# Optimization experiments

Measured on AMD Instinct MI355X. Metric: run time of the kernel, lower is better.

## Reference

```python
import jax, jax.numpy as jnp
import numpy as np

GROUPS = 4
RATIO = 2


def setup_inputs() -> dict:
    key = jax.random.key(0)
    k1, k2, k3 = jax.random.split(key, 3)
    B, C, H, W = 16, 256, 64, 64
    c_out = 2 * GROUPS * RATIO ** 2  # 32
    x = jax.random.normal(k1, (B, C, H, W), dtype=jnp.float32)
    # offset conv: normal_init std=0.001 (full 1x1 conv)
    w_off = jax.random.normal(k2, (c_out, C), dtype=jnp.float32) * 0.001
    b_off = jnp.zeros((c_out,), dtype=jnp.float32)
    # scope conv: grouped 1x1 (groups=4); init is zeros in the module, use tiny
    # random values so sigmoid != exactly 0.5 and the path is exercised
    w_scope = jax.random.normal(k3, (GROUPS, c_out // GROUPS, C // GROUPS), dtype=jnp.float32) * 0.001
    b_scope = jnp.zeros((c_out,), dtype=jnp.float32)
    return {"x": x, "w_off": w_off, "b_off": b_off, "w_scope": w_scope, "b_scope": b_scope}


def _pixel_shuffle(t, r):
    B, C, H, W = t.shape
    Co = C // (r * r)
    t = t.reshape(B, Co, r, r, H, W)
    t = t.transpose(0, 1, 4, 2, 5, 3)  # B, Co, H, r, W, r
    return t.reshape(B, Co, H * r, W * r)


def _bilinear_border(img, ix, iy):
    # img: (c, H, W); ix, iy: (Ho, Wo) pixel coords in input space
    c, H, W = img.shape
    ix = jnp.clip(ix, 0.0, W - 1.0)  # border padding: clamp coordinate
    iy = jnp.clip(iy, 0.0, H - 1.0)
    x0f = jnp.floor(ix)
    y0f = jnp.floor(iy)
    wx = ix - x0f
    wy = iy - y0f
    x0 = jnp.clip(x0f.astype(jnp.int32), 0, W - 1)
    x1 = jnp.clip(x0 + 1, 0, W - 1)
    y0 = jnp.clip(y0f.astype(jnp.int32), 0, H - 1)
    y1 = jnp.clip(y0 + 1, 0, H - 1)
    v00 = img[:, y0, x0]
    v01 = img[:, y0, x1]
    v10 = img[:, y1, x0]
    v11 = img[:, y1, x1]
    return (v00 * (1 - wy) * (1 - wx) + v01 * (1 - wy) * wx
            + v10 * wy * (1 - wx) + v11 * wy * wx)


def reference(x, w_off, b_off, w_scope, b_scope):
    B, C, H, W = x.shape
    g, r = GROUPS, RATIO
    # offset 1x1 conv
    off = jnp.einsum('bihw,oi->bohw', x, w_off) + b_off[None, :, None, None]
    # grouped scope 1x1 conv + sigmoid scaling
    xgc = x.reshape(B, g, C // g, H, W)
    sc = jnp.einsum('bgihw,goi->bgohw', xgc, w_scope).reshape(B, -1, H, W)
    sc = sc + b_scope[None, :, None, None]
    off = jax.nn.sigmoid(sc) * 0.5 * off
    # pixel shuffle to (B, 2*g, Ho, Wo)
    off = _pixel_shuffle(off, r)
    Ho, Wo = H * r, W * r
    # rearrange: x 'b (c grp) h w -> (b grp) c h w'; offset 'b (grp two) h w -> (b grp) h w two'
    cg = C // g
    xg = x.reshape(B, cg, g, H, W).transpose(0, 2, 1, 3, 4).reshape(B * g, cg, H, W)
    og = off.reshape(B, g, 2, Ho, Wo).transpose(0, 1, 3, 4, 2).reshape(B * g, Ho, Wo, 2)
    # sampling grid: centers + offset, normalized by (Wo, Ho), align_corners=False
    posx = jnp.linspace(0.5, Wo - 0.5, Wo, dtype=x.dtype)[None, :]   # (1, Wo)
    posy = jnp.linspace(0.5, Ho - 0.5, Ho, dtype=x.dtype)[:, None]   # (Ho, 1)
    gx = 2.0 * (posx + og[..., 0]) / Wo - 1.0  # (B*g, Ho, Wo)
    gy = 2.0 * (posy + og[..., 1]) / Ho - 1.0
    # unnormalize (align_corners=False): pix = ((g+1)*size - 1) / 2
    ix = ((gx + 1.0) * W - 1.0) * 0.5
    iy = ((gy + 1.0) * H - 1.0) * 0.5
    out = jax.vmap(_bilinear_border)(xg, ix, iy)  # (B*g, cg, Ho, Wo)
    # rearrange back: '(b grp) c h w -> b (c grp) h w'
    out = out.reshape(B, g, cg, Ho, Wo).transpose(0, 2, 1, 3, 4).reshape(B, C, Ho, Wo)
    return out
```

## Files before the change

### kernel.cpp

```cpp
#include <hip/hip_runtime.h>
#include <math.h>

#define B_   16
#define C_   256
#define H_   64
#define W_   64
#define G_   4
#define HO_  128
#define WO_  128
#define HW_  (H_ * W_)
#define HOWO_ (HO_ * WO_)

__global__ __launch_bounds__(256) void prep_kernel(
    const float* __restrict__ w_off,
    const float* __restrict__ w_scope,
    float* __restrict__ wcomb)
{
    const int k = blockIdx.x * 256 + threadIdx.x;
    if (k >= 4 * 64 * 40) return;
    const int q = k % 40;
    const int r = k / 40;
    const int i2 = r & 63;
    const int t  = r >> 6;
    float v;
    if (q < 32) v = w_off[q * 256 + t * 64 + i2];
    else        v = w_scope[t * 512 + (q - 32) * 64 + i2];
    wcomb[k] = v;
}

__global__ __launch_bounds__(256) void fused_kernel(
    const float* __restrict__ x,
    const float* __restrict__ wcomb,
    const float* __restrict__ b_off,
    const float* __restrict__ b_scope,
    float* __restrict__ out)
{
    __shared__ float red[4 * 64 * 32];
    __shared__ float2 coords[4 * 2 * 128];

    const int tid = threadIdx.x;
    const int t = __builtin_amdgcn_readfirstlane(tid >> 6);
    const int w = tid & 63;
    const int h = blockIdx.x & 63;
    const int b = blockIdx.x >> 6;

    const float* xq = x + (size_t)b * C_ * HW_ + (size_t)t * 64 * HW_ +
                      h * W_ + w;
    const float* wt = wcomb + t * (64 * 40);

    float aoff[32];
    float asc[8];
#pragma unroll
    for (int o = 0; o < 32; ++o) aoff[o] = 0.f;
#pragma unroll
    for (int o = 0; o < 8; ++o) asc[o] = 0.f;

#pragma unroll 2
    for (int i2 = 0; i2 < 64; ++i2) {
        const float xv = xq[(size_t)i2 * HW_];
        const float* wr = wt + i2 * 40;
#pragma unroll
        for (int o = 0; o < 32; ++o) aoff[o] += xv * wr[o];
#pragma unroll
        for (int j = 0; j < 8; ++j)  asc[j] += xv * wr[32 + j];
    }

    {
        float4* rw = (float4*)&red[(t * 64 + w) * 32];
#pragma unroll
        for (int j = 0; j < 8; ++j) {
            rw[(j + w) & 7] = make_float4(aoff[4 * j + 0], aoff[4 * j + 1],
                                          aoff[4 * j + 2], aoff[4 * j + 3]);
        }
    }
    __syncthreads();

    float4 s0 = make_float4(0.f, 0.f, 0.f, 0.f);
    float4 s1 = make_float4(0.f, 0.f, 0.f, 0.f);
#pragma unroll
    for (int tt = 0; tt < 4; ++tt) {
        const float4* rr = (const float4*)&red[(tt * 64 + w) * 32];
        const float4 a = rr[(2 * t + 0 + w) & 7];
        const float4 c = rr[(2 * t + 1 + w) & 7];
        s0.x += a.x; s0.y += a.y; s0.z += a.z; s0.w += a.w;
        s1.x += c.x; s1.y += c.y; s1.z += c.z; s1.w += c.w;
    }

    float f[8];
    {
        float ao[8] = {s0.x, s0.y, s0.z, s0.w, s1.x, s1.y, s1.z, s1.w};
#pragma unroll
        for (int j = 0; j < 8; ++j) {
            const float offv = ao[j] + b_off[8 * t + j];
            const float scv  = asc[j] + b_scope[8 * t + j];
            const float sg   = 1.f / (1.f + expf(-scv));
            f[j] = sg * 0.5f * offv;
        }
    }

#pragma unroll
    for (int r1 = 0; r1 < 2; ++r1) {
        float c2[4];
#pragma unroll
        for (int r2 = 0; r2 < 2; ++r2) {
            const int ho = 2 * h + r1;
            const int wo = 2 * w + r2;
            float ix = ((float)wo - 0.5f + f[2 * r1 + r2]) * 0.5f;
            float iy = ((float)ho - 0.5f + f[4 + 2 * r1 + r2]) * 0.5f;
            ix = fminf(fmaxf(ix, 0.f), (float)(W_ - 1));
            iy = fminf(fmaxf(iy, 0.f), (float)(H_ - 1));
            c2[2 * r2 + 0] = ix;
            c2[2 * r2 + 1] = iy;
        }
        float4* cw = (float4*)&coords[t * 256 + r1 * 128 + 2 * w];
        *cw = make_float4(c2[0], c2[1], c2[2], c2[3]);
    }

    __syncthreads();

    const int wo = tid & 127;
    const int z  = tid >> 7;
    const int ho = 2 * h + z;

    const float* xb0 = x + (size_t)b * C_ * HW_;
    float* ob0 = out + (size_t)b * C_ * HOWO_ + ho * WO_ + wo;

#pragma unroll
    for (int g = 0; g < 4; ++g) {
        const float2 c = coords[g * 256 + z * 128 + wo];
        const float ix = c.x, iy = c.y;

        const float x0f = floorf(ix);
        const float y0f = floorf(iy);
        const float wx = ix - x0f;
        const float wy = iy - y0f;
        int x0 = (int)x0f;
        int y0 = (int)y0f;
        x0 = max(0, min(x0, W_ - 1));
        y0 = max(0, min(y0, H_ - 1));
        const int x1 = min(x0 + 1, W_ - 1);
        const int y1 = min(y0 + 1, H_ - 1);

        const float w00 = (1.f - wy) * (1.f - wx);
        const float w01 = (1.f - wy) * wx;
        const float w10 = wy * (1.f - wx);
        const float w11 = wy * wx;

        const int p00 = y0 * W_ + x0;
        const int p01 = y0 * W_ + x1;
        const int p10 = y1 * W_ + x0;
        const int p11 = y1 * W_ + x1;

        const float* xb = xb0 + (size_t)g * HW_;
        float* ob = ob0 + (size_t)g * HOWO_;

#pragma unroll 4
        for (int cc = 0; cc < 64; ++cc) {
            const float* pl = xb + (size_t)cc * 4 * HW_;
            const float v = pl[p00] * w00 + pl[p01] * w01 +
                            pl[p10] * w10 + pl[p11] * w11;
            ob[(size_t)cc * 4 * HOWO_] = v;
        }
    }
}

extern "C" void kernel_launch(void* const* d_in, const int* in_sizes, int n_in,
                              void* d_out, int out_size, void* d_ws, size_t ws_size,
                              hipStream_t stream) {
    const float* x       = (const float*)d_in[0];
    const float* w_off   = (const float*)d_in[1];
    const float* b_off   = (const float*)d_in[2];
    const float* w_scope = (const float*)d_in[3];
    const float* b_scope = (const float*)d_in[4];
    float* out = (float*)d_out;
    float* wcomb = (float*)d_ws;

    prep_kernel<<<dim3(40), 256, 0, stream>>>(w_off, w_scope, wcomb);
    fused_kernel<<<dim3(B_ * H_), 256, 0, stream>>>(
        x, wcomb, b_off, b_scope, out);
}
```

Baseline: 93.94 us.

## Split fused kernel into conv and sampling kernels with global coords buffer

Splits the fused conv+sample kernel into three launches: weight prep, a conv kernel that writes sampling coordinates to global workspace, and a separate sample kernel with a 3D grid over (row pair, group, batch). The conv kernel drops the shared-memory cross-wave reduction. Each wave now reads all 256 input channels for its own 8 offset outputs, which quadruples x reads in the conv stage instead of using an LDS reduction. The sample kernel has one group per block, giving more, smaller blocks for latency hiding. The cost is an extra launch and a global round trip for the coordinates.

```diff
diff --git a/kernel.cpp b/kernel.cpp
--- a/kernel.cpp
+++ b/kernel.cpp
@@ -17,85 +17,72 @@
     float* __restrict__ wcomb)
 {
     const int k = blockIdx.x * 256 + threadIdx.x;
-    if (k >= 4 * 64 * 40) return;
-    const int q = k % 40;
-    const int r = k / 40;
-    const int i2 = r & 63;
-    const int t  = r >> 6;
+    const int q = k & 15;
+    const int i = (k >> 4) & 255;
+    const int t = k >> 12;
     float v;
-    if (q < 32) v = w_off[q * 256 + t * 64 + i2];
-    else        v = w_scope[t * 512 + (q - 32) * 64 + i2];
+    if (q < 8) {
+        v = w_off[(8 * t + q) * 256 + i];
+    } else {
+        const int i2 = i - 64 * t;
+        v = (i2 >= 0 && i2 < 64) ? w_scope[t * 512 + (q - 8) * 64 + i2] : 0.f;
+    }
     wcomb[k] = v;
 }
 
-__global__ __launch_bounds__(256) void fused_kernel(
+__global__ __launch_bounds__(256) void conv_kernel(
     const float* __restrict__ x,
     const float* __restrict__ wcomb,
     const float* __restrict__ b_off,
     const float* __restrict__ b_scope,
-    float* __restrict__ out)
+    float2* __restrict__ coords)
 {
-    __shared__ float red[4 * 64 * 32];
-    __shared__ float2 coords[4 * 2 * 128];
-
     const int tid = threadIdx.x;
     const int t = __builtin_amdgcn_readfirstlane(tid >> 6);
     const int w = tid & 63;
     const int h = blockIdx.x & 63;
     const int b = blockIdx.x >> 6;
 
-    const float* xq = x + (size_t)b * C_ * HW_ + (size_t)t * 64 * HW_ +
-                      h * W_ + w;
-    const float* wt = wcomb + t * (64 * 40);
+    const float* xrow = x + (size_t)b * C_ * HW_ + h * W_ + w;
+    const float* wt = wcomb + t * (256 * 16);
 
-    float aoff[32];
-    float asc[8];
+    float off[8];
+    float sc[8];
 #pragma unroll
-    for (int o = 0; o < 32; ++o) aoff[o] = 0.f;
+    for (int j = 0; j < 8; ++j) { off[j] = 0.f; sc[j] = 0.f; }
+
 #pragma unroll
-    for (int o = 0; o < 8; ++o) asc[o] = 0.f;
-
-#pragma unroll 2
-    for (int i2 = 0; i2 < 64; ++i2) {
-        const float xv = xq[(size_t)i2 * HW_];
-        const float* wr = wt + i2 * 40;
+    for (int seg = 0; seg < 4; ++seg) {
+        const float* xs = xrow + (size_t)seg * 64 * HW_;
+        const float* ws = wt + seg * 64 * 16;
+        if (seg == t) {
+#pragma unroll 4
+            for (int i2 = 0; i2 < 64; ++i2) {
+                const float xv = xs[(size_t)i2 * HW_];
+                const float* wr = ws + i2 * 16;
 #pragma unroll
-        for (int o = 0; o < 32; ++o) aoff[o] += xv * wr[o];
+                for (int j = 0; j < 8; ++j) off[j] += xv * wr[j];
 #pragma unroll
-        for (int j = 0; j < 8; ++j)  asc[j] += xv * wr[32 + j];
-    }
-
-    {
-        float4* rw = (float4*)&red[(t * 64 + w) * 32];
+                for (int j = 0; j < 8; ++j) sc[j] += xv * wr[8 + j];
+            }
+        } else {
+#pragma unroll 4
+            for (int i2 = 0; i2 < 64; ++i2) {
+                const float xv = xs[(size_t)i2 * HW_];
+                const float* wr = ws + i2 * 16;
 #pragma unroll
-        for (int j = 0; j < 8; ++j) {
-            rw[(j + w) & 7] = make_float4(aoff[4 * j + 0], aoff[4 * j + 1],
-                                          aoff[4 * j + 2], aoff[4 * j + 3]);
+                for (int j = 0; j < 8; ++j) off[j] += xv * wr[j];
+            }
         }
-    }
-    __syncthreads();
-
-    float4 s0 = make_float4(0.f, 0.f, 0.f, 0.f);
-    float4 s1 = make_float4(0.f, 0.f, 0.f, 0.f);
-#pragma unroll
-    for (int tt = 0; tt < 4; ++tt) {
-        const float4* rr = (const float4*)&red[(tt * 64 + w) * 32];
-        const float4 a = rr[(2 * t + 0 + w) & 7];
-        const float4 c = rr[(2 * t + 1 + w) & 7];
-        s0.x += a.x; s0.y += a.y; s0.z += a.z; s0.w += a.w;
-        s1.x += c.x; s1.y += c.y; s1.z += c.z; s1.w += c.w;
     }
 
     float f[8];
-    {
-        float ao[8] = {s0.x, s0.y, s0.z, s0.w, s1.x, s1.y, s1.z, s1.w};
 #pragma unroll
-        for (int j = 0; j < 8; ++j) {
-            const float offv = ao[j] + b_off[8 * t + j];
-            const float scv  = asc[j] + b_scope[8 * t + j];
-            const float sg   = 1.f / (1.f + expf(-scv));
-            f[j] = sg * 0.5f * offv;
-        }
+    for (int j = 0; j < 8; ++j) {
+        const float offv = off[j] + b_off[8 * t + j];
+        const float scv  = sc[j] + b_scope[8 * t + j];
+        const float sg   = 1.f / (1.f + expf(-scv));
+        f[j] = sg * 0.5f * offv;
     }
 
 #pragma unroll
@@ -112,55 +99,56 @@
             c2[2 * r2 + 0] = ix;
             c2[2 * r2 + 1] = iy;
         }
-        float4* cw = (float4*)&coords[t * 256 + r1 * 128 + 2 * w];
+        float4* cw = (float4*)&coords[(((size_t)b * G_ + t) * HO_ +
+                                       (2 * h + r1)) * WO_ + 2 * w];
         *cw = make_float4(c2[0], c2[1], c2[2], c2[3]);
     }
+}
 
-    __syncthreads();
+__global__ __launch_bounds__(256) void sample_kernel(
+    const float* __restrict__ x,
+    const float2* __restrict__ coords,
+    float* __restrict__ out)
+{
+    const int wo = threadIdx.x & 127;
+    const int ho = (blockIdx.x << 1) + (threadIdx.x >> 7);
+    const int g  = blockIdx.y;
+    const int b  = blockIdx.z;
 
-    const int wo = tid & 127;
-    const int z  = tid >> 7;
-    const int ho = 2 * h + z;
+    const float2 c = coords[(((size_t)b * G_ + g) * HO_ + ho) * WO_ + wo];
+    const float ix = c.x, iy = c.y;
 
-    const float* xb0 = x + (size_t)b * C_ * HW_;
-    float* ob0 = out + (size_t)b * C_ * HOWO_ + ho * WO_ + wo;
+    const float x0f = floorf(ix);
+    const float y0f = floorf(iy);
+    const float wx = ix - x0f;
+    const float wy = iy - y0f;
+    int x0 = (int)x0f;
+    int y0 = (int)y0f;
+    x0 = max(0, min(x0, W_ - 1));
+    y0 = max(0, min(y0, H_ - 1));
+    const int x1 = min(x0 + 1, W_ - 1);
+    const int y1 = min(y0 + 1, H_ - 1);
 
-#pragma unroll
-    for (int g = 0; g < 4; ++g) {
-        const float2 c = coords[g * 256 + z * 128 + wo];
-        const float ix = c.x, iy = c.y;
+    const float w00 = (1.f - wy) * (1.f - wx);
+    const float w01 = (1.f - wy) * wx;
+    const float w10 = wy * (1.f - wx);
+    const float w11 = wy * wx;
 
-        const float x0f = floorf(ix);
-        const float y0f = floorf(iy);
-        const float wx = ix - x0f;
-        const float wy = iy - y0f;
-        int x0 = (int)x0f;
-        int y0 = (int)y0f;
-        x0 = max(0, min(x0, W_ - 1));
-        y0 = max(0, min(y0, H_ - 1));
-        const int x1 = min(x0 + 1, W_ - 1);
-        const int y1 = min(y0 + 1, H_ - 1);
+    const int p00 = y0 * W_ + x0;
+    const int p01 = y0 * W_ + x1;
+    const int p10 = y1 * W_ + x0;
+    const int p11 = y1 * W_ + x1;
 
-        const float w00 = (1.f - wy) * (1.f - wx);
-        const float w01 = (1.f - wy) * wx;
-        const float w10 = wy * (1.f - wx);
-        const float w11 = wy * wx;
-
-        const int p00 = y0 * W_ + x0;
-        const int p01 = y0 * W_ + x1;
-        const int p10 = y1 * W_ + x0;
-        const int p11 = y1 * W_ + x1;
-
-        const float* xb = xb0 + (size_t)g * HW_;
-        float* ob = ob0 + (size_t)g * HOWO_;
+    const float* xb = x + (size_t)b * C_ * HW_ + (size_t)g * HW_;
+    float* ob = out + (size_t)b * C_ * HOWO_ + (size_t)g * HOWO_ +
+                ho * WO_ + wo;
 
 #pragma unroll 4
-        for (int cc = 0; cc < 64; ++cc) {
-            const float* pl = xb + (size_t)cc * 4 * HW_;
-            const float v = pl[p00] * w00 + pl[p01] * w01 +
-                            pl[p10] * w10 + pl[p11] * w11;
-            ob[(size_t)cc * 4 * HOWO_] = v;
-        }
+    for (int cc = 0; cc < 64; ++cc) {
+        const float* pl = xb + (size_t)cc * 4 * HW_;
+        const float v = pl[p00] * w00 + pl[p01] * w01 +
+                        pl[p10] * w10 + pl[p11] * w11;
+        ob[(size_t)cc * 4 * HOWO_] = v;
     }
 }
 
@@ -173,9 +161,12 @@
     const float* w_scope = (const float*)d_in[3];
     const float* b_scope = (const float*)d_in[4];
     float* out = (float*)d_out;
+
     float* wcomb = (float*)d_ws;
+    float2* coords = (float2*)((char*)d_ws + 65536);
 
-    prep_kernel<<<dim3(40), 256, 0, stream>>>(w_off, w_scope, wcomb);
-    fused_kernel<<<dim3(B_ * H_), 256, 0, stream>>>(
-        x, wcomb, b_off, b_scope, out);
+    prep_kernel<<<dim3(64), 256, 0, stream>>>(w_off, w_scope, wcomb);
+    conv_kernel<<<dim3(B_ * H_), 256, 0, stream>>>(
+        x, wcomb, b_off, b_scope, coords);
+    sample_kernel<<<dim3(HO_ / 2, G_, B_), 256, 0, stream>>>(x, coords, out);
 }
```

New measurement: 107.3 us. 1.14x slower.

## Double block size and split channel reduction and gather groups across 512 threads

Applied to the files above, without the earlier changes.

Blocks grow from 256 to 512 threads. Each wave of the 1x1 offset and scope projections now reduces 32 input channels instead of 64, and the partial sums are combined through a two-stage shared-memory reduction. In the sampling phase each thread handles 2 groups instead of 4, which doubles the threads issuing gather loads per row and raises memory-level parallelism. The cost is an extra barrier, more shared memory, and a launch bound of 6 that may limit registers.

```diff
diff --git a/kernel.cpp b/kernel.cpp
--- a/kernel.cpp
+++ b/kernel.cpp
@@ -17,117 +17,133 @@
     float* __restrict__ wcomb)
 {
     const int k = blockIdx.x * 256 + threadIdx.x;
-    if (k >= 4 * 64 * 40) return;
-    const int q = k % 40;
-    const int r = k / 40;
-    const int i2 = r & 63;
-    const int t  = r >> 6;
-    float v;
-    if (q < 32) v = w_off[q * 256 + t * 64 + i2];
-    else        v = w_scope[t * 512 + (q - 32) * 64 + i2];
-    wcomb[k] = v;
+    if (k >= 8 * 32 * 40) return;
+    const int q  = k % 40;
+    const int r  = k / 40;
+    const int i2 = r & 31;
+    const int u  = r >> 5;
+    const int v  = u & 3;
+    const int hi = u >> 2;
+    const int i  = 64 * v + 32 * hi + i2;
+    float val;
+    if (q < 32) val = w_off[q * 256 + i];
+    else        val = w_scope[v * 512 + (q - 32) * 64 + 32 * hi + i2];
+    wcomb[k] = val;
 }
 
-__global__ __launch_bounds__(256) void fused_kernel(
+__global__ __launch_bounds__(512, 6) void fused_kernel(
     const float* __restrict__ x,
     const float* __restrict__ wcomb,
     const float* __restrict__ b_off,
     const float* __restrict__ b_scope,
     float* __restrict__ out)
 {
-    __shared__ float red[4 * 64 * 32];
-    __shared__ float2 coords[4 * 2 * 128];
+    __shared__ float4 red[8][8][64];
+    __shared__ float4 aux[8][64];
 
     const int tid = threadIdx.x;
-    const int t = __builtin_amdgcn_readfirstlane(tid >> 6);
-    const int w = tid & 63;
-    const int h = blockIdx.x & 63;
-    const int b = blockIdx.x >> 6;
+    const int u   = __builtin_amdgcn_readfirstlane(tid >> 6);
+    const int w   = tid & 63;
+    const int v   = u & 3;
+    const int hi  = u >> 2;
+    const int h   = blockIdx.x & 63;
+    const int b   = blockIdx.x >> 6;
 
-    const float* xq = x + (size_t)b * C_ * HW_ + (size_t)t * 64 * HW_ +
-                      h * W_ + w;
-    const float* wt = wcomb + t * (64 * 40);
+    const float* xq = x + (size_t)b * C_ * HW_ +
+                      (size_t)(64 * v + 32 * hi) * HW_ + h * W_ + w;
+    const float* wt = wcomb + u * (32 * 40);
 
-    float aoff[32];
-    float asc[8];
+    float offp[32];
+    float scp[8];
 #pragma unroll
-    for (int o = 0; o < 32; ++o) aoff[o] = 0.f;
+    for (int j = 0; j < 32; ++j) offp[j] = 0.f;
 #pragma unroll
-    for (int o = 0; o < 8; ++o) asc[o] = 0.f;
+    for (int j = 0; j < 8; ++j) scp[j] = 0.f;
 
-#pragma unroll 2
-    for (int i2 = 0; i2 < 64; ++i2) {
+#pragma unroll 4
+    for (int i2 = 0; i2 < 32; ++i2) {
         const float xv = xq[(size_t)i2 * HW_];
         const float* wr = wt + i2 * 40;
 #pragma unroll
-        for (int o = 0; o < 32; ++o) aoff[o] += xv * wr[o];
+        for (int j = 0; j < 32; ++j) offp[j] += xv * wr[j];
 #pragma unroll
-        for (int j = 0; j < 8; ++j)  asc[j] += xv * wr[32 + j];
+        for (int j = 0; j < 8; ++j)  scp[j] += xv * wr[32 + j];
     }
 
-    {
-        float4* rw = (float4*)&red[(t * 64 + w) * 32];
+    if (hi) {
+#pragma unroll
+        for (int j = 0; j < 8; ++j)
+            red[4 + v][j][w] = make_float4(offp[4 * j + 0], offp[4 * j + 1],
+                                           offp[4 * j + 2], offp[4 * j + 3]);
+        aux[2 * v + 0][w] = make_float4(scp[0], scp[1], scp[2], scp[3]);
+        aux[2 * v + 1][w] = make_float4(scp[4], scp[5], scp[6], scp[7]);
+    }
+    __syncthreads();
+    if (!hi) {
 #pragma unroll
         for (int j = 0; j < 8; ++j) {
-            rw[(j + w) & 7] = make_float4(aoff[4 * j + 0], aoff[4 * j + 1],
-                                          aoff[4 * j + 2], aoff[4 * j + 3]);
+            const float4 p = red[4 + v][j][w];
+            offp[4 * j + 0] += p.x; offp[4 * j + 1] += p.y;
+            offp[4 * j + 2] += p.z; offp[4 * j + 3] += p.w;
+        }
+        const float4 s0 = aux[2 * v + 0][w];
+        const float4 s1 = aux[2 * v + 1][w];
+        scp[0] += s0.x; scp[1] += s0.y; scp[2] += s0.z; scp[3] += s0.w;
+        scp[4] += s1.x; scp[5] += s1.y; scp[6] += s1.z; scp[7] += s1.w;
+#pragma unroll
+        for (int j = 0; j < 8; ++j)
+            red[v][j][w] = make_float4(offp[4 * j + 0], offp[4 * j + 1],
+                                       offp[4 * j + 2], offp[4 * j + 3]);
+    }
+    __syncthreads();
+    if (!hi) {
+        float4 a = make_float4(0.f, 0.f, 0.f, 0.f);
+        float4 c = make_float4(0.f, 0.f, 0.f, 0.f);
+#pragma unroll
+        for (int tt = 0; tt < 4; ++tt) {
+            const float4 pa = red[tt][2 * v + 0][w];
+            const float4 pc = red[tt][2 * v + 1][w];
+            a.x += pa.x; a.y += pa.y; a.z += pa.z; a.w += pa.w;
+            c.x += pc.x; c.y += pc.y; c.z += pc.z; c.w += pc.w;
+        }
+        const float ao[8] = {a.x, a.y, a.z, a.w, c.x, c.y, c.z, c.w};
+        float f[8];
+#pragma unroll
+        for (int j = 0; j < 8; ++j) {
+            const float offv = ao[j] + b_off[8 * v + j];
+            const float scv  = scp[j] + b_scope[8 * v + j];
+            f[j] = offv * 0.5f / (1.f + expf(-scv));
+        }
+#pragma unroll
+        for (int r1 = 0; r1 < 2; ++r1) {
+            const float hoF = (float)(2 * h + r1);
+            float ix0 = ((float)(2 * w + 0) - 0.5f + f[2 * r1 + 0]) * 0.5f;
+            float iy0 = (hoF - 0.5f + f[4 + 2 * r1 + 0]) * 0.5f;
+            float ix1 = ((float)(2 * w + 1) - 0.5f + f[2 * r1 + 1]) * 0.5f;
+            float iy1 = (hoF - 0.5f + f[4 + 2 * r1 + 1]) * 0.5f;
+            ix0 = fminf(fmaxf(ix0, 0.f), (float)(W_ - 1));
+            iy0 = fminf(fmaxf(iy0, 0.f), (float)(H_ - 1));
+            ix1 = fminf(fmaxf(ix1, 0.f), (float)(W_ - 1));
+            iy1 = fminf(fmaxf(iy1, 0.f), (float)(H_ - 1));
+            aux[2 * v + r1][w] = make_float4(ix0, iy0, ix1, iy1);
         }
     }
     __syncthreads();
 
-    float4 s0 = make_float4(0.f, 0.f, 0.f, 0.f);
-    float4 s1 = make_float4(0.f, 0.f, 0.f, 0.f);
-#pragma unroll
-    for (int tt = 0; tt < 4; ++tt) {
-        const float4* rr = (const float4*)&red[(tt * 64 + w) * 32];
-        const float4 a = rr[(2 * t + 0 + w) & 7];
-        const float4 c = rr[(2 * t + 1 + w) & 7];
-        s0.x += a.x; s0.y += a.y; s0.z += a.z; s0.w += a.w;
-        s1.x += c.x; s1.y += c.y; s1.z += c.z; s1.w += c.w;
-    }
-
-    float f[8];
-    {
-        float ao[8] = {s0.x, s0.y, s0.z, s0.w, s1.x, s1.y, s1.z, s1.w};
-#pragma unroll
-        for (int j = 0; j < 8; ++j) {
-            const float offv = ao[j] + b_off[8 * t + j];
-            const float scv  = asc[j] + b_scope[8 * t + j];
-            const float sg   = 1.f / (1.f + expf(-scv));
-            f[j] = sg * 0.5f * offv;
-        }
-    }
-
-#pragma unroll
-    for (int r1 = 0; r1 < 2; ++r1) {
-        float c2[4];
-#pragma unroll
-        for (int r2 = 0; r2 < 2; ++r2) {
-            const int ho = 2 * h + r1;
-            const int wo = 2 * w + r2;
-            float ix = ((float)wo - 0.5f + f[2 * r1 + r2]) * 0.5f;
-            float iy = ((float)ho - 0.5f + f[4 + 2 * r1 + r2]) * 0.5f;
-            ix = fminf(fmaxf(ix, 0.f), (float)(W_ - 1));
-            iy = fminf(fmaxf(iy, 0.f), (float)(H_ - 1));
-            c2[2 * r2 + 0] = ix;
-            c2[2 * r2 + 1] = iy;
-        }
-        float4* cw = (float4*)&coords[t * 256 + r1 * 128 + 2 * w];
-        *cw = make_float4(c2[0], c2[1], c2[2], c2[3]);
-    }
-
-    __syncthreads();
-
     const int wo = tid & 127;
-    const int z  = tid >> 7;
+    const int q  = tid >> 7;
+    const int z  = q & 1;
+    const int gh = q >> 1;
     const int ho = 2 * h + z;
 
+    const float2* cbase = (const float2*)&aux[0][0];
     const float* xb0 = x + (size_t)b * C_ * HW_;
     float* ob0 = out + (size_t)b * C_ * HOWO_ + ho * WO_ + wo;
 
 #pragma unroll
-    for (int g = 0; g < 4; ++g) {
-        const float2 c = coords[g * 256 + z * 128 + wo];
+    for (int gg = 0; gg < 2; ++gg) {
+        const int g = 2 * gh + gg;
+        const float2 c = cbase[(g * 2 + z) * 128 + wo];
         const float ix = c.x, iy = c.y;
 
         const float x0f = floorf(ix);
@@ -157,9 +173,9 @@
 #pragma unroll 4
         for (int cc = 0; cc < 64; ++cc) {
             const float* pl = xb + (size_t)cc * 4 * HW_;
-            const float v = pl[p00] * w00 + pl[p01] * w01 +
-                            pl[p10] * w10 + pl[p11] * w11;
-            ob[(size_t)cc * 4 * HOWO_] = v;
+            const float val = pl[p00] * w00 + pl[p01] * w01 +
+                              pl[p10] * w10 + pl[p11] * w11;
+            ob[(size_t)cc * 4 * HOWO_] = val;
         }
     }
 }
@@ -176,6 +192,6 @@
     float* wcomb = (float*)d_ws;
 
     prep_kernel<<<dim3(40), 256, 0, stream>>>(w_off, w_scope, wcomb);
-    fused_kernel<<<dim3(B_ * H_), 256, 0, stream>>>(
+    fused_kernel<<<dim3(B_ * H_), 512, 0, stream>>>(
         x, wcomb, b_off, b_scope, out);
 }
```

After: 93.66 us. About the same (-0.3%).
